# Kernel optimization log

Measured on AMD Instinct MI355X. Metric: run time of the kernel, lower is better.

Reference implementation:

```python
import jax, jax.numpy as jnp
import numpy as np

WINDOW_SIZE = 7
CHANNEL = 1
SIGMA = 1.5


def _create_window(window_size=WINDOW_SIZE, channel=CHANNEL):
    coords = jnp.arange(window_size, dtype=jnp.float32) - window_size // 2
    g = jnp.exp(-coords ** 2 / (2.0 * SIGMA ** 2))
    g = g / g.sum()
    w2d = g[:, None] * g[None, :]                      # [K, K]
    # depthwise kernel, OIHW with I=1 (groups=channel)
    return jnp.broadcast_to(w2d[None, None], (channel, 1, window_size, window_size))


def _dwconv(x, window):
    pad = WINDOW_SIZE // 2
    return jax.lax.conv_general_dilated(
        x, window,
        window_strides=(1, 1),
        padding=[(pad, pad), (pad, pad)],
        dimension_numbers=('NCHW', 'OIHW', 'NCHW'),
        feature_group_count=CHANNEL,
    )


def setup_inputs() -> dict:
    key = jax.random.key(0)
    k1, k2 = jax.random.split(key)
    shape = (128, CHANNEL, 256, 256)
    pred = jax.random.uniform(k1, shape, dtype=jnp.float32)
    target = jax.random.uniform(k2, shape, dtype=jnp.float32)
    window = _create_window()
    return {"pred": pred, "target": target, "window": window}


def reference(pred, target, window):
    C1 = 0.01 ** 2
    C2 = 0.03 ** 2
    mu1 = _dwconv(pred, window)
    mu2 = _dwconv(target, window)
    mu1_sq = mu1 * mu1
    mu2_sq = mu2 * mu2
    mu12 = mu1 * mu2
    sigma1_sq = _dwconv(pred * pred, window) - mu1_sq
    sigma2_sq = _dwconv(target * target, window) - mu2_sq
    sigma12 = _dwconv(pred * target, window) - mu12
    ssim_map = ((2.0 * mu12 + C1) * (2.0 * sigma12 + C2)) / (
        (mu1_sq + mu2_sq + C1) * (sigma1_sq + sigma2_sq + C2))
    return 1.0 - ssim_map.mean()
```

## Files before the change

### kernel.cpp

```cpp
#include <hip/hip_runtime.h>

#define IMG_H 256
#define IMG_W 256
#define ROWS 16
#define NIMG 128
#define NWAVES (NIMG * 64)

__device__ __forceinline__ float ssim1(float mu1, float mu2, float spp, float stt, float spt) {
    const float C1 = 1e-4f, C2 = 9e-4f;
    float mu1s = mu1 * mu1, mu2s = mu2 * mu2, mu12 = mu1 * mu2;
    float s1 = spp - mu1s, s2 = stt - mu2s, s12 = spt - mu12;
    float num = (2.f * mu12 + C1) * (2.f * s12 + C2);
    float den = (mu1s + mu2s + C1) * (s1 + s2 + C2);
    return num * __builtin_amdgcn_rcpf(den);
}

template<int ATOMIC>
__global__ __launch_bounds__(256) void ssim_main(
    const float* __restrict__ pred,
    const float* __restrict__ targ,
    const float* __restrict__ window,
    float* __restrict__ wsum)
{
    __shared__ float2 sbuf[4][72];

    const int lane = threadIdx.x & 63;
    const int wid  = threadIdx.x >> 6;
    const int gw   = blockIdx.x * 4 + wid;
    const int n    = gw >> 6;
    const int r    = gw & 63;
    const int r0   = (r >> 2) * ROWS;
    const int X0   = (r & 3) << 6;

    float g[7];
    {
        float sum = 0.f;
#pragma unroll
        for (int j = 0; j < 7; ++j) { g[j] = window[21 + j]; sum += g[j]; }
        float inv = 1.f / sum;
#pragma unroll
        for (int j = 0; j < 7; ++j) g[j] *= inv;
    }

    const float* pimg = pred + (size_t)n * (IMG_H * IMG_W);
    const float* timg = targ + (size_t)n * (IMG_H * IMG_W);
    const int mo = X0 + lane;

    int hidx = 0, hcol = 0;
    if (lane < 3)      { hidx = lane + 1;  hcol = X0 - 3 + lane;  }
    else if (lane < 6) { hidx = lane + 65; hcol = X0 + 61 + lane; }
    const bool hv = (lane < 6) && ((unsigned)hcol < (unsigned)IMG_W);

    float Amu[7], Atu[7], App[7], Att[7], Apt[7];
    float acc = 0.f;

    float Pr, Tr;
    float2 Hr;

#define GLOAD(J) { \
    const int j_ = (J); \
    Pr = 0.f; Tr = 0.f; Hr = make_float2(0.f, 0.f); \
    if ((unsigned)j_ < (unsigned)IMG_H) { \
        Pr = pimg[j_ * IMG_W + mo]; \
        Tr = timg[j_ * IMG_W + mo]; \
        if (hv) { \
            Hr.x = pimg[j_ * IMG_W + hcol]; \
            Hr.y = timg[j_ * IMG_W + hcol]; \
        } \
    } }

#define TAP(K, P, T) { \
    float wp = g[K] * (P), wt = g[K] * (T); \
    m_  = fmaf(g[K], (P), m_);  u_  = fmaf(g[K], (T), u_); \
    pp_ = fmaf(wp, (P), pp_);   tt_ = fmaf(wt, (T), tt_); \
    pt_ = fmaf(wp, (T), pt_); }

#define VD(A_, U) ( fmaf(g[6], A_[((U)+6)%7], fmaf(g[5], A_[((U)+5)%7], \
    fmaf(g[4], A_[((U)+4)%7], fmaf(g[3], A_[((U)+3)%7], fmaf(g[2], A_[((U)+2)%7], \
    fmaf(g[1], A_[((U)+1)%7], g[0] * A_[(U)%7])))))) )

#define OUTR(U) { \
    float m1 = VD(Amu,U), m2 = VD(Atu,U), pp = VD(App,U), tt = VD(Att,U), pt = VD(Apt,U); \
    acc += ssim1(m1, m2, pp, tt, pt); }

#define STEPX(SLOT, JOFF, HASOUT, U, DOLOAD) { \
    { \
        float2* sw = sbuf[wid]; \
        sw[lane + 4] = make_float2(Pr, Tr); \
        if (lane < 6) sw[hidx] = Hr; \
    } \
    const float2* sb = sbuf[wid]; \
    float2 q0 = sb[lane + 1], q1 = sb[lane + 2], q2 = sb[lane + 3]; \
    float2 q3 = sb[lane + 4], q4 = sb[lane + 5], q5 = sb[lane + 6]; \
    float2 q6 = sb[lane + 7]; \
    if (DOLOAD) { GLOAD(r0 + (JOFF) + 1); } \
    { \
        float m_ = 0.f, u_ = 0.f, pp_ = 0.f, tt_ = 0.f, pt_ = 0.f; \
        TAP(0, q0.x, q0.y) TAP(1, q1.x, q1.y) TAP(2, q2.x, q2.y) \
        TAP(3, q3.x, q3.y) TAP(4, q4.x, q4.y) TAP(5, q5.x, q5.y) \
        TAP(6, q6.x, q6.y) \
        Amu[SLOT] = m_; Atu[SLOT] = u_; App[SLOT] = pp_; \
        Att[SLOT] = tt_; Apt[SLOT] = pt_; \
    } \
    if (HASOUT) { OUTR(U) } }

    GLOAD(r0 - 3);

    STEPX(0, -3, 0, 0, 1)
    STEPX(1, -2, 0, 0, 1)
    STEPX(2, -1, 0, 0, 1)
    STEPX(3,  0, 0, 0, 1)
    STEPX(4,  1, 0, 0, 1)
    STEPX(5,  2, 0, 0, 1)

#pragma unroll 1
    for (int jb = 0; jb < 2; ++jb) {
        const int base = 3 + jb * 7;
        STEPX(6, base,     1, 0, 1)
        STEPX(0, base + 1, 1, 1, 1)
        STEPX(1, base + 2, 1, 2, 1)
        STEPX(2, base + 3, 1, 3, 1)
        STEPX(3, base + 4, 1, 4, 1)
        STEPX(4, base + 5, 1, 5, 1)
        STEPX(5, base + 6, 1, 6, 1)
    }
    STEPX(6, 17, 1, 0, 1)
    STEPX(0, 18, 1, 1, 0)

#undef GLOAD
#undef TAP
#undef VD
#undef OUTR
#undef STEPX

#pragma unroll
    for (int off = 32; off > 0; off >>= 1)
        acc += __shfl_xor(acc, off, 64);
    if (lane == 0) {
        if (ATOMIC) atomicAdd(&wsum[0], acc);
        else        wsum[gw] = acc;
    }
}

__global__ __launch_bounds__(256) void ssim_final_arr(
    const float* __restrict__ ws, float* __restrict__ out)
{
    __shared__ double sred[4];
    double sm = 0.0;
#pragma unroll
    for (int k = 0; k < NWAVES / 256; ++k)
        sm += (double)ws[threadIdx.x + k * 256];
#pragma unroll
    for (int off = 32; off > 0; off >>= 1)
        sm += __shfl_down(sm, off, 64);
    const int lane = threadIdx.x & 63, wid = threadIdx.x >> 6;
    if (lane == 0) sred[wid] = sm;
    __syncthreads();
    if (threadIdx.x == 0) {
        double tot = sred[0] + sred[1] + sred[2] + sred[3];
        out[0] = (float)(1.0 - tot * (1.0 / (128.0 * 256.0 * 256.0)));
    }
}

__global__ void ssim_final_sc(const float* __restrict__ ws, float* __restrict__ out)
{
    out[0] = 1.0f - ws[0] * (1.0f / (128.0f * 256.0f * 256.0f));
}

extern "C" void kernel_launch(void* const* d_in, const int* in_sizes, int n_in,
                              void* d_out, int out_size, void* d_ws, size_t ws_size,
                              hipStream_t stream)
{
    const float* pred   = (const float*)d_in[0];
    const float* targ   = (const float*)d_in[1];
    const float* window = (const float*)d_in[2];
    float* out = (float*)d_out;
    float* ws  = (float*)d_ws;

    if (ws_size >= NWAVES * sizeof(float)) {
        ssim_main<0><<<NWAVES / 4, 256, 0, stream>>>(pred, targ, window, ws);
        ssim_final_arr<<<1, 256, 0, stream>>>(ws, out);
    } else {
        hipMemsetAsync(ws, 0, sizeof(float), stream);
        ssim_main<1><<<NWAVES / 4, 256, 0, stream>>>(pred, targ, window, ws);
        ssim_final_sc<<<1, 1, 0, stream>>>(ws, out);
    }
    (void)in_sizes; (void)n_in; (void)out_size;
}
```

Measured before the change: 44.64 us.

## Double-buffer LDS row reads and use 8-slot ring for vertical accumulators

Reads the next row's seven shared-memory taps into a second register set while the current row's horizontal taps are computed from the previous set. The shared-memory load latency then overlaps with arithmetic. The vertical ring buffer grows from 7 to 8 slots, which lets the loop cover 16 output rows in two 8-step iterations with power-of-two indexing and drops the tail steps. It costs about 14 extra float2 registers plus 5 more accumulator slots, so register pressure and occupancy may get worse.

```diff
diff --git a/kernel.cpp b/kernel.cpp
--- a/kernel.cpp
+++ b/kernel.cpp
@@ -51,11 +51,15 @@
     else if (lane < 6) { hidx = lane + 65; hcol = X0 + 61 + lane; }
     const bool hv = (lane < 6) && ((unsigned)hcol < (unsigned)IMG_W);
 
-    float Amu[7], Atu[7], App[7], Att[7], Apt[7];
+    float Amu[8], Atu[8], App[8], Att[8], Apt[8];
+    float2 qA[7], qB[7];
     float acc = 0.f;
 
     float Pr, Tr;
     float2 Hr;
+
+    float2* sw       = sbuf[wid];
+    const float2* sb = sbuf[wid];
 
 #define GLOAD(J) { \
     const int j_ = (J); \
@@ -69,67 +73,69 @@
         } \
     } }
 
-#define TAP(K, P, T) { \
-    float wp = g[K] * (P), wt = g[K] * (T); \
-    m_  = fmaf(g[K], (P), m_);  u_  = fmaf(g[K], (T), u_); \
-    pp_ = fmaf(wp, (P), pp_);   tt_ = fmaf(wt, (T), tt_); \
-    pt_ = fmaf(wp, (T), pt_); }
+#define TAP(K, Q) { \
+    float p = (Q).x, t = (Q).y; \
+    float wp = g[K] * p, wt = g[K] * t; \
+    m_  = fmaf(g[K], p, m_);  u_  = fmaf(g[K], t, u_); \
+    pp_ = fmaf(wp, p, pp_);   tt_ = fmaf(wt, t, tt_); \
+    pt_ = fmaf(wp, t, pt_); }
 
-#define VD(A_, U) ( fmaf(g[6], A_[((U)+6)%7], fmaf(g[5], A_[((U)+5)%7], \
-    fmaf(g[4], A_[((U)+4)%7], fmaf(g[3], A_[((U)+3)%7], fmaf(g[2], A_[((U)+2)%7], \
-    fmaf(g[1], A_[((U)+1)%7], g[0] * A_[(U)%7])))))) )
+#define VD8(A_, VB) ( fmaf(g[6], A_[((VB)+6)&7], fmaf(g[5], A_[((VB)+5)&7], \
+    fmaf(g[4], A_[((VB)+4)&7], fmaf(g[3], A_[((VB)+3)&7], fmaf(g[2], A_[((VB)+2)&7], \
+    fmaf(g[1], A_[((VB)+1)&7], g[0] * A_[(VB)&7])))))) )
 
-#define OUTR(U) { \
-    float m1 = VD(Amu,U), m2 = VD(Atu,U), pp = VD(App,U), tt = VD(Att,U), pt = VD(Apt,U); \
+#define OUTR(VB) { \
+    float m1 = VD8(Amu,VB), m2 = VD8(Atu,VB), pp = VD8(App,VB), \
+          tt = VD8(Att,VB), pt = VD8(Apt,VB); \
     acc += ssim1(m1, m2, pp, tt, pt); }
 
-#define STEPX(SLOT, JOFF, HASOUT, U, DOLOAD) { \
-    { \
-        float2* sw = sbuf[wid]; \
-        sw[lane + 4] = make_float2(Pr, Tr); \
-        if (lane < 6) sw[hidx] = Hr; \
-    } \
-    const float2* sb = sbuf[wid]; \
-    float2 q0 = sb[lane + 1], q1 = sb[lane + 2], q2 = sb[lane + 3]; \
-    float2 q3 = sb[lane + 4], q4 = sb[lane + 5], q5 = sb[lane + 6]; \
-    float2 q6 = sb[lane + 7]; \
-    if (DOLOAD) { GLOAD(r0 + (JOFF) + 1); } \
+#define STEPX(SLOT, QC, QN, JNEXT, HASOUT, VB, DOLOAD) { \
+    sw[lane + 4] = make_float2(Pr, Tr); \
+    if (lane < 6) sw[hidx] = Hr; \
+    QN[0] = sb[lane + 1]; QN[1] = sb[lane + 2]; QN[2] = sb[lane + 3]; \
+    QN[3] = sb[lane + 4]; QN[4] = sb[lane + 5]; QN[5] = sb[lane + 6]; \
+    QN[6] = sb[lane + 7]; \
+    if (DOLOAD) { GLOAD(JNEXT); } \
     { \
         float m_ = 0.f, u_ = 0.f, pp_ = 0.f, tt_ = 0.f, pt_ = 0.f; \
-        TAP(0, q0.x, q0.y) TAP(1, q1.x, q1.y) TAP(2, q2.x, q2.y) \
-        TAP(3, q3.x, q3.y) TAP(4, q4.x, q4.y) TAP(5, q5.x, q5.y) \
-        TAP(6, q6.x, q6.y) \
+        TAP(0, QC[0]) TAP(1, QC[1]) TAP(2, QC[2]) TAP(3, QC[3]) \
+        TAP(4, QC[4]) TAP(5, QC[5]) TAP(6, QC[6]) \
         Amu[SLOT] = m_; Atu[SLOT] = u_; App[SLOT] = pp_; \
         Att[SLOT] = tt_; Apt[SLOT] = pt_; \
     } \
-    if (HASOUT) { OUTR(U) } }
+    if (HASOUT) { OUTR(VB) } }
 
     GLOAD(r0 - 3);
+    sw[lane + 4] = make_float2(Pr, Tr);
+    if (lane < 6) sw[hidx] = Hr;
+    qA[0] = sb[lane + 1]; qA[1] = sb[lane + 2]; qA[2] = sb[lane + 3];
+    qA[3] = sb[lane + 4]; qA[4] = sb[lane + 5]; qA[5] = sb[lane + 6];
+    qA[6] = sb[lane + 7];
+    GLOAD(r0 - 2);
 
-    STEPX(0, -3, 0, 0, 1)
-    STEPX(1, -2, 0, 0, 1)
-    STEPX(2, -1, 0, 0, 1)
-    STEPX(3,  0, 0, 0, 1)
-    STEPX(4,  1, 0, 0, 1)
-    STEPX(5,  2, 0, 0, 1)
+    STEPX(0, qA, qB, r0 - 1, 0, 0, 1)
+    STEPX(1, qB, qA, r0,     0, 0, 1)
+    STEPX(2, qA, qB, r0 + 1, 0, 0, 1)
+    STEPX(3, qB, qA, r0 + 2, 0, 0, 1)
+    STEPX(4, qA, qB, r0 + 3, 0, 0, 1)
+    STEPX(5, qB, qA, r0 + 4, 0, 0, 1)
 
 #pragma unroll 1
     for (int jb = 0; jb < 2; ++jb) {
-        const int base = 3 + jb * 7;
-        STEPX(6, base,     1, 0, 1)
-        STEPX(0, base + 1, 1, 1, 1)
-        STEPX(1, base + 2, 1, 2, 1)
-        STEPX(2, base + 3, 1, 3, 1)
-        STEPX(3, base + 4, 1, 4, 1)
-        STEPX(4, base + 5, 1, 5, 1)
-        STEPX(5, base + 6, 1, 6, 1)
+        const int jbase = r0 + 5 + jb * 8;
+        STEPX(6, qA, qB, jbase,     1, 0, 1)
+        STEPX(7, qB, qA, jbase + 1, 1, 1, 1)
+        STEPX(0, qA, qB, jbase + 2, 1, 2, 1)
+        STEPX(1, qB, qA, jbase + 3, 1, 3, 1)
+        STEPX(2, qA, qB, jbase + 4, 1, 4, 1)
+        STEPX(3, qB, qA, jbase + 5, 1, 5, 1)
+        STEPX(4, qA, qB, jbase + 6, 1, 6, 1)
+        STEPX(5, qB, qA, jbase + 7, 1, 7, 1)
     }
-    STEPX(6, 17, 1, 0, 1)
-    STEPX(0, 18, 1, 1, 0)
 
 #undef GLOAD
 #undef TAP
-#undef VD
+#undef VD8
 #undef OUTR
 #undef STEPX
 
```

After: 55.87 us. 25.2% more time.

## Process two 64-column strips per wavefront to halve wave count

Applied to the files above, without the earlier changes.

Each wavefront now handles two adjacent 64-column strips (128 columns) of a 16-row band instead of one. Wave count and the number of partial sums are halved, and the two independent strips interleave loads and FMAs to raise instruction-level parallelism. In exchange, register pressure doubles (two sets of 35 accumulators) and there is half as much wave-level parallelism, which may lower occupancy.

```diff
diff --git a/kernel.cpp b/kernel.cpp
--- a/kernel.cpp
+++ b/kernel.cpp
@@ -4,7 +4,7 @@
 #define IMG_W 256
 #define ROWS 16
 #define NIMG 128
-#define NWAVES (NIMG * 64)
+#define NWAVES 4096
 
 __device__ __forceinline__ float ssim1(float mu1, float mu2, float spp, float stt, float spt) {
     const float C1 = 1e-4f, C2 = 9e-4f;
@@ -22,15 +22,17 @@
     const float* __restrict__ window,
     float* __restrict__ wsum)
 {
-    __shared__ float2 sbuf[4][72];
+    __shared__ float2 sbuf[8][72];
 
     const int lane = threadIdx.x & 63;
     const int wid  = threadIdx.x >> 6;
     const int gw   = blockIdx.x * 4 + wid;
-    const int n    = gw >> 6;
-    const int r    = gw & 63;
-    const int r0   = (r >> 2) * ROWS;
-    const int X0   = (r & 3) << 6;
+    const int n    = gw >> 5;
+    const int r    = gw & 31;
+    const int r0   = (r >> 1) * ROWS;
+    const int qh   = r & 1;
+    const int X0a  = qh << 7;
+    const int X0b  = X0a + 64;
 
     float g[7];
     {
@@ -44,94 +46,109 @@
 
     const float* pimg = pred + (size_t)n * (IMG_H * IMG_W);
     const float* timg = targ + (size_t)n * (IMG_H * IMG_W);
-    const int mo = X0 + lane;
-
-    int hidx = 0, hcol = 0;
-    if (lane < 3)      { hidx = lane + 1;  hcol = X0 - 3 + lane;  }
-    else if (lane < 6) { hidx = lane + 65; hcol = X0 + 61 + lane; }
-    const bool hv = (lane < 6) && ((unsigned)hcol < (unsigned)IMG_W);
-
-    float Amu[7], Atu[7], App[7], Att[7], Apt[7];
+    const int moA = X0a + lane;
+    const int moB = X0b + lane;
+
+    int hidx = 0, hoff = 0;
+    if (lane < 3)      { hidx = lane + 1;  hoff = lane - 3; }
+    else if (lane < 6) { hidx = lane + 65; hoff = lane + 61; }
+    const int hcolA = X0a + hoff, hcolB = X0b + hoff;
+    const bool hvA = (lane < 6) && ((unsigned)hcolA < (unsigned)IMG_W);
+    const bool hvB = (lane < 6) && ((unsigned)hcolB < (unsigned)IMG_W);
+
+    float AmuA[7], AtuA[7], AppA[7], AttA[7], AptA[7];
+    float AmuB[7], AtuB[7], AppB[7], AttB[7], AptB[7];
     float acc = 0.f;
 
-    float Pr, Tr;
-    float2 Hr;
-
-#define GLOAD(J) { \
+    float PrA, TrA, PrB, TrB;
+    float2 HrA, HrB;
+
+    float2* swA       = sbuf[wid * 2];
+    float2* swB       = sbuf[wid * 2 + 1];
+    const float2* sbA = swA;
+    const float2* sbB = swB;
+
+#define GLOADD(J) { \
     const int j_ = (J); \
-    Pr = 0.f; Tr = 0.f; Hr = make_float2(0.f, 0.f); \
+    PrA = 0.f; TrA = 0.f; PrB = 0.f; TrB = 0.f; \
+    HrA = make_float2(0.f, 0.f); HrB = HrA; \
     if ((unsigned)j_ < (unsigned)IMG_H) { \
-        Pr = pimg[j_ * IMG_W + mo]; \
-        Tr = timg[j_ * IMG_W + mo]; \
-        if (hv) { \
-            Hr.x = pimg[j_ * IMG_W + hcol]; \
-            Hr.y = timg[j_ * IMG_W + hcol]; \
-        } \
+        const int rb = j_ * IMG_W; \
+        PrA = pimg[rb + moA]; TrA = timg[rb + moA]; \
+        PrB = pimg[rb + moB]; TrB = timg[rb + moB]; \
+        if (hvA) { HrA.x = pimg[rb + hcolA]; HrA.y = timg[rb + hcolA]; } \
+        if (hvB) { HrB.x = pimg[rb + hcolB]; HrB.y = timg[rb + hcolB]; } \
     } }
 
-#define TAP(K, P, T) { \
-    float wp = g[K] * (P), wt = g[K] * (T); \
-    m_  = fmaf(g[K], (P), m_);  u_  = fmaf(g[K], (T), u_); \
-    pp_ = fmaf(wp, (P), pp_);   tt_ = fmaf(wt, (T), tt_); \
-    pt_ = fmaf(wp, (T), pt_); }
+#define TAP(K, Q) { \
+    float p = (Q).x, t = (Q).y; \
+    float wp = g[K] * p, wt = g[K] * t; \
+    m_  = fmaf(g[K], p, m_);  u_  = fmaf(g[K], t, u_); \
+    pp_ = fmaf(wp, p, pp_);   tt_ = fmaf(wt, t, tt_); \
+    pt_ = fmaf(wp, t, pt_); }
+
+#define HCQ(SLOT, MU, TU, PP, TT, PT, Q0, Q1, Q2, Q3, Q4, Q5, Q6) { \
+    float m_ = 0.f, u_ = 0.f, pp_ = 0.f, tt_ = 0.f, pt_ = 0.f; \
+    TAP(0, Q0) TAP(1, Q1) TAP(2, Q2) TAP(3, Q3) \
+    TAP(4, Q4) TAP(5, Q5) TAP(6, Q6) \
+    MU[SLOT] = m_; TU[SLOT] = u_; PP[SLOT] = pp_; \
+    TT[SLOT] = tt_; PT[SLOT] = pt_; }
 
 #define VD(A_, U) ( fmaf(g[6], A_[((U)+6)%7], fmaf(g[5], A_[((U)+5)%7], \
     fmaf(g[4], A_[((U)+4)%7], fmaf(g[3], A_[((U)+3)%7], fmaf(g[2], A_[((U)+2)%7], \
     fmaf(g[1], A_[((U)+1)%7], g[0] * A_[(U)%7])))))) )
 
-#define OUTR(U) { \
-    float m1 = VD(Amu,U), m2 = VD(Atu,U), pp = VD(App,U), tt = VD(Att,U), pt = VD(Apt,U); \
+#define OUTQ(U, MU, TU, PP, TT, PT) { \
+    float m1 = VD(MU,U), m2 = VD(TU,U), pp = VD(PP,U), \
+          tt = VD(TT,U), pt = VD(PT,U); \
     acc += ssim1(m1, m2, pp, tt, pt); }
 
-#define STEPX(SLOT, JOFF, HASOUT, U, DOLOAD) { \
-    { \
-        float2* sw = sbuf[wid]; \
-        sw[lane + 4] = make_float2(Pr, Tr); \
-        if (lane < 6) sw[hidx] = Hr; \
-    } \
-    const float2* sb = sbuf[wid]; \
-    float2 q0 = sb[lane + 1], q1 = sb[lane + 2], q2 = sb[lane + 3]; \
-    float2 q3 = sb[lane + 4], q4 = sb[lane + 5], q5 = sb[lane + 6]; \
-    float2 q6 = sb[lane + 7]; \
-    if (DOLOAD) { GLOAD(r0 + (JOFF) + 1); } \
-    { \
-        float m_ = 0.f, u_ = 0.f, pp_ = 0.f, tt_ = 0.f, pt_ = 0.f; \
-        TAP(0, q0.x, q0.y) TAP(1, q1.x, q1.y) TAP(2, q2.x, q2.y) \
-        TAP(3, q3.x, q3.y) TAP(4, q4.x, q4.y) TAP(5, q5.x, q5.y) \
-        TAP(6, q6.x, q6.y) \
-        Amu[SLOT] = m_; Atu[SLOT] = u_; App[SLOT] = pp_; \
-        Att[SLOT] = tt_; Apt[SLOT] = pt_; \
-    } \
-    if (HASOUT) { OUTR(U) } }
-
-    GLOAD(r0 - 3);
-
-    STEPX(0, -3, 0, 0, 1)
-    STEPX(1, -2, 0, 0, 1)
-    STEPX(2, -1, 0, 0, 1)
-    STEPX(3,  0, 0, 0, 1)
-    STEPX(4,  1, 0, 0, 1)
-    STEPX(5,  2, 0, 0, 1)
+#define STEPD(SLOT, JOFF, HASOUT, U, DOLOAD) { \
+    swA[lane + 4] = make_float2(PrA, TrA); \
+    if (lane < 6) swA[hidx] = HrA; \
+    float2 a0 = sbA[lane + 1], a1 = sbA[lane + 2], a2 = sbA[lane + 3], \
+           a3 = sbA[lane + 4], a4 = sbA[lane + 5], a5 = sbA[lane + 6], \
+           a6 = sbA[lane + 7]; \
+    swB[lane + 4] = make_float2(PrB, TrB); \
+    if (lane < 6) swB[hidx] = HrB; \
+    float2 b0 = sbB[lane + 1], b1 = sbB[lane + 2], b2 = sbB[lane + 3], \
+           b3 = sbB[lane + 4], b4 = sbB[lane + 5], b5 = sbB[lane + 6], \
+           b6 = sbB[lane + 7]; \
+    if (DOLOAD) { GLOADD(r0 + (JOFF) + 1); } \
+    HCQ(SLOT, AmuA, AtuA, AppA, AttA, AptA, a0, a1, a2, a3, a4, a5, a6) \
+    if (HASOUT) { OUTQ(U, AmuA, AtuA, AppA, AttA, AptA) } \
+    HCQ(SLOT, AmuB, AtuB, AppB, AttB, AptB, b0, b1, b2, b3, b4, b5, b6) \
+    if (HASOUT) { OUTQ(U, AmuB, AtuB, AppB, AttB, AptB) } }
+
+    GLOADD(r0 - 3);
+
+    STEPD(0, -3, 0, 0, 1)
+    STEPD(1, -2, 0, 0, 1)
+    STEPD(2, -1, 0, 0, 1)
+    STEPD(3,  0, 0, 0, 1)
+    STEPD(4,  1, 0, 0, 1)
+    STEPD(5,  2, 0, 0, 1)
 
 #pragma unroll 1
     for (int jb = 0; jb < 2; ++jb) {
         const int base = 3 + jb * 7;
-        STEPX(6, base,     1, 0, 1)
-        STEPX(0, base + 1, 1, 1, 1)
-        STEPX(1, base + 2, 1, 2, 1)
-        STEPX(2, base + 3, 1, 3, 1)
-        STEPX(3, base + 4, 1, 4, 1)
-        STEPX(4, base + 5, 1, 5, 1)
-        STEPX(5, base + 6, 1, 6, 1)
-    }
-    STEPX(6, 17, 1, 0, 1)
-    STEPX(0, 18, 1, 1, 0)
-
-#undef GLOAD
+        STEPD(6, base,     1, 0, 1)
+        STEPD(0, base + 1, 1, 1, 1)
+        STEPD(1, base + 2, 1, 2, 1)
+        STEPD(2, base + 3, 1, 3, 1)
+        STEPD(3, base + 4, 1, 4, 1)
+        STEPD(4, base + 5, 1, 5, 1)
+        STEPD(5, base + 6, 1, 6, 1)
+    }
+    STEPD(6, 17, 1, 0, 1)
+    STEPD(0, 18, 1, 1, 0)
+
+#undef GLOADD
 #undef TAP
+#undef HCQ
 #undef VD
-#undef OUTR
-#undef STEPX
+#undef OUTQ
+#undef STEPD
 
 #pragma unroll
     for (int off = 32; off > 0; off >>= 1)
```

Measured after the change: 70.63 us. +58.2%, slower.

## Stage rows directly into LDS with global_load_lds and exploit kernel symmetry

Applied to the files above, without the earlier changes.

Replaces register-staged global loads followed by LDS writes with direct global-to-LDS async loads into a double buffer, including halo columns, with explicit vmcnt waits. It also folds the symmetric Gaussian taps so the horizontal and vertical passes need fewer multiplies, and splits pred/target into separate planar LDS rows instead of float2. The goal is to cut VGPR pressure and the LDS write instructions. In exchange it takes on an s_waitcnt vmcnt(0) full drain every step and relies on the window being symmetric.

```diff
diff --git a/kernel.cpp b/kernel.cpp
--- a/kernel.cpp
+++ b/kernel.cpp
@@ -4,7 +4,14 @@
 #define IMG_W 256
 #define ROWS 16
 #define NIMG 128
-#define NWAVES (NIMG * 64)
+#define NWAVES (NIMG * 16 * 4)
+
+typedef const __attribute__((address_space(1))) float ga_f32;
+typedef __attribute__((address_space(3))) float ls_f32;
+
+__device__ __forceinline__ void gll(const float* g, float* l) {
+    __builtin_amdgcn_global_load_lds((ga_f32*)g, (ls_f32*)l, 4, 0, 0);
+}
 
 __device__ __forceinline__ float ssim1(float mu1, float mu2, float spp, float stt, float spt) {
     const float C1 = 1e-4f, C2 = 9e-4f;
@@ -22,7 +29,7 @@
     const float* __restrict__ window,
     float* __restrict__ wsum)
 {
-    __shared__ float2 sbuf[4][72];
+    __shared__ float sbuf[4][2][140];
 
     const int lane = threadIdx.x & 63;
     const int wid  = threadIdx.x >> 6;
@@ -32,90 +39,108 @@
     const int r0   = (r >> 2) * ROWS;
     const int X0   = (r & 3) << 6;
 
-    float g[7];
+    float g0, g1, g2, g3;
     {
-        float sum = 0.f;
-#pragma unroll
-        for (int j = 0; j < 7; ++j) { g[j] = window[21 + j]; sum += g[j]; }
-        float inv = 1.f / sum;
-#pragma unroll
-        for (int j = 0; j < 7; ++j) g[j] *= inv;
+        float w0 = window[21], w1 = window[22], w2 = window[23], w3 = window[24],
+              w4 = window[25], w5 = window[26], w6 = window[27];
+        float inv = 1.f / (((w0 + w6) + (w1 + w5)) + ((w2 + w4) + w3));
+        g0 = w0 * inv; g1 = w1 * inv; g2 = w2 * inv; g3 = w3 * inv;
     }
 
     const float* pimg = pred + (size_t)n * (IMG_H * IMG_W);
     const float* timg = targ + (size_t)n * (IMG_H * IMG_W);
-    const int mo = X0 + lane;
-
-    int hidx = 0, hcol = 0;
-    if (lane < 3)      { hidx = lane + 1;  hcol = X0 - 3 + lane;  }
-    else if (lane < 6) { hidx = lane + 65; hcol = X0 + 61 + lane; }
-    const bool hv = (lane < 6) && ((unsigned)hcol < (unsigned)IMG_W);
+    const int mo  = X0 + lane;
+    const int hco = (lane < 3) ? (X0 - 3 + lane) : (X0 + 61 + lane);
+    const bool lval = (X0 > 0);
+    const bool rval = (X0 < 192);
 
     float Amu[7], Atu[7], App[7], Att[7], Apt[7];
     float acc = 0.f;
 
-    float Pr, Tr;
-    float2 Hr;
-
-#define GLOAD(J) { \
+    float* br = &sbuf[wid][0][0];
+    float* bw = &sbuf[wid][1][0];
+
+    if (!lval && lane < 3) {
+        br[lane] = 0.f; br[70 + lane] = 0.f;
+        bw[lane] = 0.f; bw[70 + lane] = 0.f;
+    }
+    if (!rval && lane >= 3 && lane < 6) {
+        br[64 + lane] = 0.f; br[134 + lane] = 0.f;
+        bw[64 + lane] = 0.f; bw[134 + lane] = 0.f;
+    }
+
+#define STAGE(BW, J) { \
     const int j_ = (J); \
-    Pr = 0.f; Tr = 0.f; Hr = make_float2(0.f, 0.f); \
     if ((unsigned)j_ < (unsigned)IMG_H) { \
-        Pr = pimg[j_ * IMG_W + mo]; \
-        Tr = timg[j_ * IMG_W + mo]; \
-        if (hv) { \
-            Hr.x = pimg[j_ * IMG_W + hcol]; \
-            Hr.y = timg[j_ * IMG_W + hcol]; \
+        const float* prow_ = pimg + j_ * IMG_W; \
+        const float* trow_ = timg + j_ * IMG_W; \
+        gll(prow_ + mo, (BW) + 3); \
+        gll(trow_ + mo, (BW) + 73); \
+        if (lval && lane < 3) { \
+            gll(prow_ + hco, (BW)); \
+            gll(trow_ + hco, (BW) + 70); \
+        } \
+        if (rval && lane >= 3 && lane < 6) { \
+            gll(prow_ + hco, (BW) + 64); \
+            gll(trow_ + hco, (BW) + 134); \
+        } \
+    } else { \
+        (BW)[3 + lane] = 0.f; (BW)[73 + lane] = 0.f; \
+        if (lane < 6) { \
+            const int hx_ = (lane < 3) ? lane : (64 + lane); \
+            (BW)[hx_] = 0.f; (BW)[hx_ + 70] = 0.f; \
         } \
     } }
 
-#define TAP(K, P, T) { \
-    float wp = g[K] * (P), wt = g[K] * (T); \
-    m_  = fmaf(g[K], (P), m_);  u_  = fmaf(g[K], (T), u_); \
-    pp_ = fmaf(wp, (P), pp_);   tt_ = fmaf(wt, (T), tt_); \
-    pt_ = fmaf(wp, (T), pt_); }
-
-#define VD(A_, U) ( fmaf(g[6], A_[((U)+6)%7], fmaf(g[5], A_[((U)+5)%7], \
-    fmaf(g[4], A_[((U)+4)%7], fmaf(g[3], A_[((U)+3)%7], fmaf(g[2], A_[((U)+2)%7], \
-    fmaf(g[1], A_[((U)+1)%7], g[0] * A_[(U)%7])))))) )
+#define VD(A_, U) ( fmaf(g0, A_[(U)%7] + A_[((U)+6)%7], \
+    fmaf(g1, A_[((U)+1)%7] + A_[((U)+5)%7], \
+    fmaf(g2, A_[((U)+2)%7] + A_[((U)+4)%7], g3 * A_[((U)+3)%7]))) )
 
 #define OUTR(U) { \
-    float m1 = VD(Amu,U), m2 = VD(Atu,U), pp = VD(App,U), tt = VD(Att,U), pt = VD(Apt,U); \
+    float m1 = VD(Amu,U), m2 = VD(Atu,U), pp = VD(App,U), \
+          tt = VD(Att,U), pt = VD(Apt,U); \
     acc += ssim1(m1, m2, pp, tt, pt); }
 
-#define STEPX(SLOT, JOFF, HASOUT, U, DOLOAD) { \
+#define STEPX(SLOT, JNEXT, HASOUT, U, DOSTAGE) { \
+    asm volatile("s_waitcnt vmcnt(0)" ::: "memory"); \
+    float p0 = br[lane],      p1 = br[lane + 1],  p2 = br[lane + 2], \
+          p3 = br[lane + 3],  p4 = br[lane + 4],  p5 = br[lane + 5], \
+          p6 = br[lane + 6]; \
+    float t0 = br[lane + 70], t1 = br[lane + 71], t2 = br[lane + 72], \
+          t3 = br[lane + 73], t4 = br[lane + 74], t5 = br[lane + 75], \
+          t6 = br[lane + 76]; \
+    if (DOSTAGE) { STAGE(bw, JNEXT) } \
     { \
-        float2* sw = sbuf[wid]; \
-        sw[lane + 4] = make_float2(Pr, Tr); \
-        if (lane < 6) sw[hidx] = Hr; \
+        float a, b, c, d; \
+        a = p0 + p6; b = p1 + p5; c = p2 + p4; \
+        Amu[SLOT] = fmaf(g0, a, fmaf(g1, b, fmaf(g2, c, g3 * p3))); \
+        a = t0 + t6; b = t1 + t5; c = t2 + t4; \
+        Atu[SLOT] = fmaf(g0, a, fmaf(g1, b, fmaf(g2, c, g3 * t3))); \
+        a = fmaf(p6, p6, p0 * p0); b = fmaf(p5, p5, p1 * p1); \
+        c = fmaf(p4, p4, p2 * p2); d = p3 * p3; \
+        App[SLOT] = fmaf(g0, a, fmaf(g1, b, fmaf(g2, c, g3 * d))); \
+        a = fmaf(t6, t6, t0 * t0); b = fmaf(t5, t5, t1 * t1); \
+        c = fmaf(t4, t4, t2 * t2); d = t3 * t3; \
+        Att[SLOT] = fmaf(g0, a, fmaf(g1, b, fmaf(g2, c, g3 * d))); \
+        a = fmaf(p6, t6, p0 * t0); b = fmaf(p5, t5, p1 * t1); \
+        c = fmaf(p4, t4, p2 * t2); d = p3 * t3; \
+        Apt[SLOT] = fmaf(g0, a, fmaf(g1, b, fmaf(g2, c, g3 * d))); \
     } \
-    const float2* sb = sbuf[wid]; \
-    float2 q0 = sb[lane + 1], q1 = sb[lane + 2], q2 = sb[lane + 3]; \
-    float2 q3 = sb[lane + 4], q4 = sb[lane + 5], q5 = sb[lane + 6]; \
-    float2 q6 = sb[lane + 7]; \
-    if (DOLOAD) { GLOAD(r0 + (JOFF) + 1); } \
-    { \
-        float m_ = 0.f, u_ = 0.f, pp_ = 0.f, tt_ = 0.f, pt_ = 0.f; \
-        TAP(0, q0.x, q0.y) TAP(1, q1.x, q1.y) TAP(2, q2.x, q2.y) \
-        TAP(3, q3.x, q3.y) TAP(4, q4.x, q4.y) TAP(5, q5.x, q5.y) \
-        TAP(6, q6.x, q6.y) \
-        Amu[SLOT] = m_; Atu[SLOT] = u_; App[SLOT] = pp_; \
-        Att[SLOT] = tt_; Apt[SLOT] = pt_; \
-    } \
-    if (HASOUT) { OUTR(U) } }
-
-    GLOAD(r0 - 3);
-
-    STEPX(0, -3, 0, 0, 1)
-    STEPX(1, -2, 0, 0, 1)
-    STEPX(2, -1, 0, 0, 1)
-    STEPX(3,  0, 0, 0, 1)
-    STEPX(4,  1, 0, 0, 1)
-    STEPX(5,  2, 0, 0, 1)
+    if (HASOUT) { OUTR(U) } \
+    { float* swp_ = br; br = bw; bw = swp_; } }
+
+    STAGE(br, r0 - 3)
+
+    STEPX(0, r0 - 2, 0, 0, 1)
+    STEPX(1, r0 - 1, 0, 0, 1)
+    STEPX(2, r0,     0, 0, 1)
+    STEPX(3, r0 + 1, 0, 0, 1)
+    STEPX(4, r0 + 2, 0, 0, 1)
+    STEPX(5, r0 + 3, 0, 0, 1)
 
 #pragma unroll 1
     for (int jb = 0; jb < 2; ++jb) {
-        const int base = 3 + jb * 7;
+        const int base = r0 + 4 + jb * 7;
         STEPX(6, base,     1, 0, 1)
         STEPX(0, base + 1, 1, 1, 1)
         STEPX(1, base + 2, 1, 2, 1)
@@ -124,11 +149,10 @@
         STEPX(4, base + 5, 1, 5, 1)
         STEPX(5, base + 6, 1, 6, 1)
     }
-    STEPX(6, 17, 1, 0, 1)
-    STEPX(0, 18, 1, 1, 0)
-
-#undef GLOAD
-#undef TAP
+    STEPX(6, r0 + 18, 1, 0, 1)
+    STEPX(0, 0,       1, 1, 0)
+
+#undef STAGE
 #undef VD
 #undef OUTR
 #undef STEPX
```

Result: slower. 52.17 us (+16.9%).
